# Kernel optimization log

Measured on AMD Instinct MI355X. Metric: run time of the kernel, lower is better.

## Reference

```python
import jax, jax.numpy as jnp
import numpy as np

N = 100000   # nodes
E = 3200000  # edges
C = 256      # in_channels
H = 64       # hidden_channels
G = 512      # graphs in batch
FC = [128, 64, 32, 16]
OUT = 2
EPS = 1e-5


def _linear(key, fan_in, fan_out):
    k1, k2 = jax.random.split(key)
    s = 1.0 / np.sqrt(fan_in)
    W = jax.random.uniform(k1, (fan_in, fan_out), jnp.float32, -s, s)
    b = jax.random.uniform(k2, (fan_out,), jnp.float32, -s, s)
    return W, b


def setup_inputs() -> dict:
    key = jax.random.key(0)
    ks = jax.random.split(key, 12)
    x = jax.random.normal(ks[0], (N, C), jnp.float32)
    edge_index = jax.random.randint(ks[1], (2, E), 0, N, dtype=jnp.int64)
    batch = jnp.sort(jax.random.randint(ks[2], (N,), 0, G, dtype=jnp.int64))
    w1, b1 = _linear(ks[3], C, H)
    w2, b2 = _linear(ks[4], H, H)
    g1 = jnp.ones((H,), jnp.float32); be1 = jnp.zeros((H,), jnp.float32)
    g2 = jnp.ones((H,), jnp.float32); be2 = jnp.zeros((H,), jnp.float32)
    fw1, fb1 = _linear(ks[5], H, FC[0])
    fw2, fb2 = _linear(ks[6], FC[0], FC[1])
    fw3, fb3 = _linear(ks[7], FC[1], FC[2])
    fw4, fb4 = _linear(ks[8], FC[2], FC[3])
    ow, ob = _linear(ks[9], FC[3], OUT)
    return dict(x=x, edge_index=edge_index, batch=batch,
                w1=w1, b1=b1, w2=w2, b2=b2,
                g1=g1, be1=be1, g2=g2, be2=be2,
                fw1=fw1, fb1=fb1, fw2=fw2, fb2=fb2,
                fw3=fw3, fb3=fb3, fw4=fw4, fb4=fb4,
                ow=ow, ob=ob)


def _gcn_layers(x, edge_index, w1, b1, w2, b2, g1, be1, g2, be2):
    # PyG GCNConv: add self loops, symmetric deg^-1/2 normalization, scatter-add at dst
    loops = jnp.arange(N, dtype=edge_index.dtype)
    src = jnp.concatenate([edge_index[0], loops])
    dst = jnp.concatenate([edge_index[1], loops])
    deg = jax.ops.segment_sum(jnp.ones((E + N,), jnp.float32), dst, num_segments=N)
    dis = jnp.where(deg > 0, jax.lax.rsqrt(jnp.maximum(deg, 1.0)), 0.0)
    norm = (dis[src] * dis[dst])[:, None]  # [E+N, 1]

    def conv(h, W, b):
        h = h @ W
        return jax.ops.segment_sum(h[src] * norm, dst, num_segments=N) + b

    def bn(h, g, be):  # BatchNorm1d over node dim (training-mode batch stats)
        m = jnp.mean(h, axis=0)
        v = jnp.var(h, axis=0)
        return (h - m) * jax.lax.rsqrt(v + EPS) * g + be

    h = bn(jax.nn.relu(conv(x, w1, b1)), g1, be1)   # dropout = identity (eval)
    h = bn(jax.nn.relu(conv(h, w2, b2)), g2, be2)
    return h


def reference(x, edge_index, batch, w1, b1, w2, b2, g1, be1, g2, be2,
              fw1, fb1, fw2, fb2, fw3, fb3, fw4, fb4, ow, ob):
    h = _gcn_layers(x, edge_index, w1, b1, w2, b2, g1, be1, g2, be2)
    # global_mean_pool over batch vector
    s = jax.ops.segment_sum(h, batch, num_segments=G)
    cnt = jax.ops.segment_sum(jnp.ones((N,), jnp.float32), batch, num_segments=G)
    p = s / jnp.maximum(cnt, 1.0)[:, None]  # [G, H]
    h = jax.nn.relu(p @ fw1 + fb1)
    h = jax.nn.relu(h @ fw2 + fb2)
    h = jax.nn.relu(h @ fw3 + fb3)
    h = jax.nn.relu(h @ fw4 + fb4)
    return h @ ow + ob  # [G, OUT]
```

## Files before the change

kernel.cpp:

```cpp
#include <hip/hip_runtime.h>
#include <hip/hip_fp16.h>

#define N_NODES 100000
#define E_EDGES 3200000
#define NG      512
#define BN_EPS  1e-5f

#define BSH     7
#define BNODES  128
#define NBUCK   782
#define NCHUNK  256
#define CHUNK   12500
#define DCAP    5120

__global__ __launch_bounds__(256) void k_zero(int* __restrict__ btot,
                                              float* __restrict__ stats1,
                                              float* __restrict__ stats2,
                                              float* __restrict__ sums,
                                              float* __restrict__ cnt) {
  int i = blockIdx.x * 256 + threadIdx.x;
  if (i < NBUCK) btot[i] = 0;
  if (i < 128) { stats1[i] = 0.f; stats2[i] = 0.f; }
  if (i < NG * 64) sums[i] = 0.f;
  if (i < NG) cnt[i] = 0.f;
}

__global__ __launch_bounds__(256) void kb_hist(const int* __restrict__ ei,
                                               int* __restrict__ btot) {
  __shared__ int h[NBUCK];
  const int c = blockIdx.x, tid = threadIdx.x;
  for (int b = tid; b < NBUCK; b += 256) h[b] = 0;
  __syncthreads();
  const int* dst = ei + E_EDGES + c * CHUNK;
  for (int i = tid; i < CHUNK; i += 256) atomicAdd(&h[dst[i] >> BSH], 1);
  __syncthreads();
  for (int b = tid; b < NBUCK; b += 256)
    if (h[b]) atomicAdd(&btot[b], h[b]);
}

__global__ __launch_bounds__(1024) void kb_scan2(const int* __restrict__ btot,
                                                 int* __restrict__ bbase,
                                                 int* __restrict__ cursor) {
  __shared__ int sm[1024];
  const int tid = threadIdx.x;
  const int cval = (tid < NBUCK) ? btot[tid] : 0;
  int val = cval;
  sm[tid] = val;
  __syncthreads();
  for (int off = 1; off < 1024; off <<= 1) {
    int t = (tid >= off) ? sm[tid - off] : 0;
    __syncthreads();
    val += t;
    sm[tid] = val;
    __syncthreads();
  }
  if (tid < NBUCK) { bbase[tid] = val - cval; cursor[tid] = val - cval; }
  if (tid == NBUCK - 1) bbase[NBUCK] = val;
}

__global__ __launch_bounds__(256) void kb_scatter(const int* __restrict__ ei,
                                                  int* __restrict__ cursor,
                                                  int* __restrict__ binned) {
  __shared__ int cnt[NBUCK], lcur[NBUCK], res[NBUCK];
  const int c = blockIdx.x, tid = threadIdx.x;
  for (int b = tid; b < NBUCK; b += 256) cnt[b] = 0;
  __syncthreads();
  const int* srcp = ei + c * CHUNK;
  const int* dstp = ei + E_EDGES + c * CHUNK;
  for (int i = tid; i < CHUNK; i += 256) atomicAdd(&cnt[dstp[i] >> BSH], 1);
  __syncthreads();
  for (int b = tid; b < NBUCK; b += 256) {
    res[b] = cnt[b] ? atomicAdd(&cursor[b], cnt[b]) : 0;
    lcur[b] = 0;
  }
  __syncthreads();
  for (int i = tid; i < CHUNK; i += 256) {
    const int s = srcp[i], d = dstp[i];
    const int b = d >> BSH;
    const int slot = atomicAdd(&lcur[b], 1);
    binned[res[b] + slot] = ((d & (BNODES - 1)) << 17) | s;
  }
}

__global__ __launch_bounds__(256) void kb_degsort(const int* __restrict__ binned,
                                                  const int* __restrict__ bbase,
                                                  int* __restrict__ csr,
                                                  int* __restrict__ row_start,
                                                  float* __restrict__ dis) {
  __shared__ int sA[DCAP];
  __shared__ int sB[DCAP];
  __shared__ int h[BNODES];
  __shared__ int pre[BNODES];
  __shared__ int cur[BNODES];
  const int b = blockIdx.x, tid = threadIdx.x;
  const int e0 = bbase[b], e1 = bbase[b + 1];
  const int sz = e1 - e0;
  if (tid < BNODES) h[tid] = 0;
  __syncthreads();
  if (sz <= DCAP) {
    for (int i = tid; i < sz; i += 256) {
      const int v = binned[e0 + i];
      sA[i] = v;
      atomicAdd(&h[v >> 17], 1);
    }
  } else {
    for (int i = e0 + tid; i < e1; i += 256) atomicAdd(&h[binned[i] >> 17], 1);
  }
  __syncthreads();
  if (tid < BNODES) pre[tid] = h[tid];
  __syncthreads();
  for (int off = 1; off < BNODES; off <<= 1) {
    int t = (tid >= off && tid < BNODES) ? pre[tid - off] : 0;
    __syncthreads();
    if (tid < BNODES) pre[tid] += t;
    __syncthreads();
  }
  if (tid < BNODES) {
    const int ex = pre[tid] - h[tid];
    const int n = b * BNODES + tid;
    if (n < N_NODES) {
      row_start[n] = e0 + ex;
      dis[n] = rsqrtf((float)(h[tid] + 1));
    }
    cur[tid] = ex;
  }
  if (b == NBUCK - 1 && tid == 0) row_start[N_NODES] = E_EDGES;
  __syncthreads();
  if (sz <= DCAP) {
    for (int i = tid; i < sz; i += 256) {
      const int v = sA[i];
      const int pos = atomicAdd(&cur[v >> 17], 1);
      sB[pos] = v & 0x1FFFF;
    }
    __syncthreads();
    for (int i = tid; i < sz; i += 256) csr[e0 + i] = sB[i];
  } else {
    for (int i = e0 + tid; i < e1; i += 256) {
      const int v = binned[i];
      const int pos = atomicAdd(&cur[v >> 17], 1);
      csr[e0 + pos] = v & 0x1FFFF;
    }
  }
}

template <int K, bool BN>
__global__ __launch_bounds__(256) void k_gemm(const float* __restrict__ in,
                                              const float* __restrict__ W,
                                              const float* __restrict__ dis,
                                              const float* __restrict__ stats,
                                              const float* __restrict__ gam,
                                              const float* __restrict__ bet,
                                              __half* __restrict__ y) {
  __shared__ float xs[64 * 68];
  __shared__ float wsm[64 * 64];
  __shared__ float scv[64], shv[64];
  const int tid = threadIdx.x;
  const int n0 = blockIdx.x * 64;
  const int lane = tid & 63, wv = tid >> 6;
  const int nq = lane & 15;
  const int chb = wv * 16 + (lane >> 4) * 4;
  if (BN) {
    if (tid < 64) {
      const float m = stats[tid] * (1.0f / N_NODES);
      const float v = stats[64 + tid] * (1.0f / N_NODES) - m * m;
      const float sc = rsqrtf(v + BN_EPS) * gam[tid];
      scv[tid] = sc;
      shv[tid] = bet[tid] - m * sc;
    }
  }
  float a[4][4] = {{0,0,0,0},{0,0,0,0},{0,0,0,0},{0,0,0,0}};
  for (int c0 = 0; c0 < K; c0 += 64) {
    __syncthreads();
#pragma unroll
    for (int i = 0; i < 4; ++i) {
      const int idx = tid + i * 256;
      const int n = idx >> 4, c4 = (idx & 15) * 4;
      const int nn = min(n0 + n, N_NODES - 1);
      float4 v = *(const float4*)&in[(size_t)nn * K + c0 + c4];
      if (BN) {
        v.x = v.x * scv[c4] + shv[c4];
        v.y = v.y * scv[c4 + 1] + shv[c4 + 1];
        v.z = v.z * scv[c4 + 2] + shv[c4 + 2];
        v.w = v.w * scv[c4 + 3] + shv[c4 + 3];
      }
      *(float4*)&xs[n * 68 + c4] = v;
    }
#pragma unroll
    for (int i = 0; i < 4; ++i) {
      const int idx = tid + i * 256;
      const int c = idx >> 4, ch4 = (idx & 15) * 4;
      *(float4*)&wsm[c * 64 + ch4] = *(const float4*)&W[(size_t)(c0 + c) * 64 + ch4];
    }
    __syncthreads();
    for (int c = 0; c < 64; c += 4) {
      float wq[4][4];
#pragma unroll
      for (int cc = 0; cc < 4; ++cc) {
        const float4 w4 = *(const float4*)&wsm[(c + cc) * 64 + chb];
        wq[cc][0] = w4.x; wq[cc][1] = w4.y; wq[cc][2] = w4.z; wq[cc][3] = w4.w;
      }
#pragma unroll
      for (int i = 0; i < 4; ++i) {
        const float4 xv = *(const float4*)&xs[(nq + 16 * i) * 68 + c];
#pragma unroll
        for (int j = 0; j < 4; ++j) {
          a[i][j] = fmaf(xv.x, wq[0][j],
                    fmaf(xv.y, wq[1][j],
                    fmaf(xv.z, wq[2][j],
                    fmaf(xv.w, wq[3][j], a[i][j]))));
        }
      }
    }
  }
#pragma unroll
  for (int i = 0; i < 4; ++i) {
    const int n = n0 + nq + 16 * i;
    if (n < N_NODES) {
      const float d = dis[n];
      union { __half h[4]; float2 f; } u;
      u.h[0] = __float2half_rn(d * a[i][0]);
      u.h[1] = __float2half_rn(d * a[i][1]);
      u.h[2] = __float2half_rn(d * a[i][2]);
      u.h[3] = __float2half_rn(d * a[i][3]);
      *(float2*)&y[(size_t)n * 64 + chb] = u.f;
    }
  }
}

template <bool POOL>
__global__ __launch_bounds__(256) void k_gather(const int* __restrict__ csr,
                                                const int* __restrict__ rs,
                                                const __half* __restrict__ y,
                                                const float* __restrict__ dis,
                                                const float* __restrict__ bias,
                                                float* __restrict__ hout,
                                                float* __restrict__ stats,
                                                const int* __restrict__ batch,
                                                float* __restrict__ sums,
                                                float* __restrict__ cnt) {
  const int tid = threadIdx.x;
  const int lane = tid & 63;
  const int p = lane >> 5;
  const int c = lane & 31;
  const int wid = (blockIdx.x * 256 + tid) >> 6;
  const int nw = (gridDim.x * 256) >> 6;
  const int per = (N_NODES + nw - 1) / nw;
  const int n0 = wid * per;
  const int n1 = min(N_NODES, n0 + per);
  const float bx = bias[2 * c], by = bias[2 * c + 1];
  float s1x = 0.f, s1y = 0.f, s2x = 0.f, s2y = 0.f;
  int curg = -1, run = 0;
  float px = 0.f, py = 0.f;
  for (int n = n0; n < n1; ++n) {
    int e = rs[n];
    const int end = rs[n + 1];
    float ax = 0.f, ay = 0.f;
    if (p == 0) {
      const float2 f = __half22float2(*(const __half2*)&y[(size_t)n * 64 + 2 * c]);
      ax = f.x; ay = f.y;
    }
    for (; e + 8 <= end; e += 8) {
      const int i0 = csr[e + p];
      const int i1 = csr[e + 2 + p];
      const int i2 = csr[e + 4 + p];
      const int i3 = csr[e + 6 + p];
      const float2 f0 = __half22float2(*(const __half2*)&y[(size_t)i0 * 64 + 2 * c]);
      const float2 f1 = __half22float2(*(const __half2*)&y[(size_t)i1 * 64 + 2 * c]);
      const float2 f2 = __half22float2(*(const __half2*)&y[(size_t)i2 * 64 + 2 * c]);
      const float2 f3 = __half22float2(*(const __half2*)&y[(size_t)i3 * 64 + 2 * c]);
      ax += (f0.x + f1.x) + (f2.x + f3.x);
      ay += (f0.y + f1.y) + (f2.y + f3.y);
    }
    for (; e + 2 <= end; e += 2) {
      const int i0 = csr[e + p];
      const float2 f = __half22float2(*(const __half2*)&y[(size_t)i0 * 64 + 2 * c]);
      ax += f.x; ay += f.y;
    }
    if (e < end && p == 0) {
      const int i0 = csr[e];
      const float2 f = __half22float2(*(const __half2*)&y[(size_t)i0 * 64 + 2 * c]);
      ax += f.x; ay += f.y;
    }
    ax += __shfl_xor(ax, 32);
    ay += __shfl_xor(ay, 32);
    const float d = dis[n];
    const float vx = fmaxf(d * ax + bx, 0.f);
    const float vy = fmaxf(d * ay + by, 0.f);
    if (lane < 32) {
      if (!POOL) *(float2*)&hout[(size_t)n * 64 + 2 * c] = make_float2(vx, vy);
      s1x += vx; s1y += vy;
      s2x += vx * vx; s2y += vy * vy;
    }
    if (POOL) {
      const int g = batch[n];
      if (g != curg) {
        if (run) {
          if (lane < 32) {
            atomicAdd(&sums[curg * 64 + 2 * c], px);
            atomicAdd(&sums[curg * 64 + 2 * c + 1], py);
          }
          if (lane == 0) atomicAdd(&cnt[curg], (float)run);
        }
        curg = g; run = 0; px = 0.f; py = 0.f;
      }
      if (lane < 32) { px += vx; py += vy; }
      ++run;
    }
  }
  if (POOL && run) {
    if (lane < 32) {
      atomicAdd(&sums[curg * 64 + 2 * c], px);
      atomicAdd(&sums[curg * 64 + 2 * c + 1], py);
    }
    if (lane == 0) atomicAdd(&cnt[curg], (float)run);
  }
  __shared__ float r1[256], r2[256];
  const int wv = tid >> 6;
  if (lane < 32) {
    r1[wv * 64 + 2 * c] = s1x; r1[wv * 64 + 2 * c + 1] = s1y;
    r2[wv * 64 + 2 * c] = s2x; r2[wv * 64 + 2 * c + 1] = s2y;
  }
  __syncthreads();
  if (tid < 64) {
    atomicAdd(&stats[tid], r1[tid] + r1[tid + 64] + r1[tid + 128] + r1[tid + 192]);
  } else if (tid < 128) {
    const int h = tid - 64;
    atomicAdd(&stats[64 + h], r2[h] + r2[h + 64] + r2[h + 128] + r2[h + 192]);
  }
}

__global__ __launch_bounds__(128) void k_mlp(const float* __restrict__ sums,
                                             const float* __restrict__ cnt,
                                             const float* __restrict__ stats,
                                             const float* __restrict__ gam,
                                             const float* __restrict__ bet,
                                             const float* __restrict__ fw1, const float* __restrict__ fb1,
                                             const float* __restrict__ fw2, const float* __restrict__ fb2,
                                             const float* __restrict__ fw3, const float* __restrict__ fb3,
                                             const float* __restrict__ fw4, const float* __restrict__ fb4,
                                             const float* __restrict__ ow, const float* __restrict__ ob,
                                             float* __restrict__ out) {
  __shared__ float u0[128], u1[128];
  const int g = blockIdx.x, t = threadIdx.x;
  if (t < 64) {
    const float m = stats[t] * (1.0f / N_NODES);
    const float v = stats[64 + t] * (1.0f / N_NODES) - m * m;
    const float sc = rsqrtf(v + BN_EPS) * gam[t];
    const float sh = bet[t] - m * sc;
    u0[t] = (sums[g * 64 + t] / fmaxf(cnt[g], 1.0f)) * sc + sh;
  }
  __syncthreads();
  if (t < 128) {
    float a = fb1[t];
    for (int k = 0; k < 64; ++k) a = fmaf(u0[k], fw1[k * 128 + t], a);
    u1[t] = fmaxf(a, 0.f);
  }
  __syncthreads();
  if (t < 64) {
    float a = fb2[t];
    for (int k = 0; k < 128; ++k) a = fmaf(u1[k], fw2[k * 64 + t], a);
    u0[t] = fmaxf(a, 0.f);
  }
  __syncthreads();
  if (t < 32) {
    float a = fb3[t];
    for (int k = 0; k < 64; ++k) a = fmaf(u0[k], fw3[k * 32 + t], a);
    u1[t] = fmaxf(a, 0.f);
  }
  __syncthreads();
  if (t < 16) {
    float a = fb4[t];
    for (int k = 0; k < 32; ++k) a = fmaf(u1[k], fw4[k * 16 + t], a);
    u0[t] = fmaxf(a, 0.f);
  }
  __syncthreads();
  if (t < 2) {
    float a = ob[t];
    for (int k = 0; k < 16; ++k) a = fmaf(u0[k], ow[k * 2 + t], a);
    out[g * 2 + t] = a;
  }
}

extern "C" void kernel_launch(void* const* d_in, const int* in_sizes, int n_in,
                              void* d_out, int out_size, void* d_ws, size_t ws_size,
                              hipStream_t stream) {
  const float* x    = (const float*)d_in[0];
  const int*   ei   = (const int*)d_in[1];
  const int*   batch= (const int*)d_in[2];
  const float* w1   = (const float*)d_in[3];
  const float* b1   = (const float*)d_in[4];
  const float* w2   = (const float*)d_in[5];
  const float* b2   = (const float*)d_in[6];
  const float* g1   = (const float*)d_in[7];
  const float* be1  = (const float*)d_in[8];
  const float* g2   = (const float*)d_in[9];
  const float* be2  = (const float*)d_in[10];
  const float* fw1  = (const float*)d_in[11]; const float* fb1 = (const float*)d_in[12];
  const float* fw2  = (const float*)d_in[13]; const float* fb2 = (const float*)d_in[14];
  const float* fw3  = (const float*)d_in[15]; const float* fb3 = (const float*)d_in[16];
  const float* fw4  = (const float*)d_in[17]; const float* fb4 = (const float*)d_in[18];
  const float* ow   = (const float*)d_in[19]; const float* ob  = (const float*)d_in[20];
  float* out = (float*)d_out;

  char* ws = (char*)d_ws;
  auto alloc = [&](size_t bytes) {
    void* p = ws;
    ws += (bytes + 255) & ~(size_t)255;
    return p;
  };
  float*  dis      = (float*)alloc((size_t)N_NODES * 4);
  int*    btot     = (int*)  alloc((size_t)NBUCK * 4);
  int*    bbase    = (int*)  alloc((size_t)(NBUCK + 1) * 4);
  int*    cursor   = (int*)  alloc((size_t)NBUCK * 4);
  int*    binned   = (int*)  alloc((size_t)E_EDGES * 4);
  int*    csr      = (int*)  alloc((size_t)E_EDGES * 4);
  int*    row_start= (int*)  alloc((size_t)(N_NODES + 1) * 4);
  __half* yH       = (__half*)alloc((size_t)N_NODES * 64 * 2);
  float*  hB       = (float*)alloc((size_t)N_NODES * 64 * 4);
  float*  stats1   = (float*)alloc(512);
  float*  stats2   = (float*)alloc(512);
  float*  sums     = (float*)alloc((size_t)NG * 64 * 4);
  float*  cnt      = (float*)alloc((size_t)NG * 4);

  const int nblkG = (N_NODES + 63) / 64;

  k_zero    <<<128, 256, 0, stream>>>(btot, stats1, stats2, sums, cnt);
  kb_hist   <<<NCHUNK, 256, 0, stream>>>(ei, btot);
  kb_scan2  <<<1, 1024, 0, stream>>>(btot, bbase, cursor);
  kb_scatter<<<NCHUNK, 256, 0, stream>>>(ei, cursor, binned);
  kb_degsort<<<NBUCK, 256, 0, stream>>>(binned, bbase, csr, row_start, dis);

  k_gemm<256, false><<<nblkG, 256, 0, stream>>>(x, w1, dis, nullptr, nullptr, nullptr, yH);
  k_gather<false><<<2048, 256, 0, stream>>>(csr, row_start, yH, dis, b1, hB, stats1,
                                            nullptr, nullptr, nullptr);

  k_gemm<64, true><<<nblkG, 256, 0, stream>>>(hB, w2, dis, stats1, g1, be1, yH);
  k_gather<true><<<2048, 256, 0, stream>>>(csr, row_start, yH, dis, b2, nullptr, stats2,
                                           batch, sums, cnt);

  k_mlp<<<NG, 128, 0, stream>>>(sums, cnt, stats2, g2, be2,
                                fw1, fb1, fw2, fb2, fw3, fb3, fw4, fb4, ow, ob, out);
}
```

Baseline: 610.3 us.

## Use MFMA fp16 GEMM and channel-group-major layout for gather

Moves the dense transform onto fp16 MFMA instructions, converting inputs and weights to half in shared memory. The intermediate features are stored channel-group-major (8 groups of 8 channels per node), and the gather kernel is split so each block handles one channel group, with 16 edges processed in parallel per wave. The aim is a smaller per-group working set that fits in cache during the random neighbour gather. It also halves the hidden buffer by storing it in fp16. The cost is that each edge index is reread 8 times, and precision drops for the input and hidden activations.

```diff
diff --git a/kernel.cpp b/kernel.cpp
--- a/kernel.cpp
+++ b/kernel.cpp
@@ -12,6 +12,9 @@
 #define NCHUNK  256
 #define CHUNK   12500
 #define DCAP    5120
+
+typedef _Float16 h8 __attribute__((ext_vector_type(8)));
+typedef float f4 __attribute__((ext_vector_type(4)));
 
 __global__ __launch_bounds__(256) void k_zero(int* __restrict__ btot,
                                               float* __restrict__ stats1,
@@ -144,85 +147,107 @@
 }
 
 template <int K, bool BN>
-__global__ __launch_bounds__(256) void k_gemm(const float* __restrict__ in,
+__global__ __launch_bounds__(256) void k_gemm(const void* __restrict__ in_,
                                               const float* __restrict__ W,
                                               const float* __restrict__ dis,
                                               const float* __restrict__ stats,
                                               const float* __restrict__ gam,
                                               const float* __restrict__ bet,
                                               __half* __restrict__ y) {
-  __shared__ float xs[64 * 68];
-  __shared__ float wsm[64 * 64];
+  __shared__ _Float16 xs[64 * 72];
+  __shared__ _Float16 wt[64 * 72];
   __shared__ float scv[64], shv[64];
   const int tid = threadIdx.x;
+  const int lane = tid & 63, wv = tid >> 6;
+  const int quad = lane >> 4, mrow = lane & 15;
   const int n0 = blockIdx.x * 64;
-  const int lane = tid & 63, wv = tid >> 6;
-  const int nq = lane & 15;
-  const int chb = wv * 16 + (lane >> 4) * 4;
-  if (BN) {
-    if (tid < 64) {
-      const float m = stats[tid] * (1.0f / N_NODES);
-      const float v = stats[64 + tid] * (1.0f / N_NODES) - m * m;
-      const float sc = rsqrtf(v + BN_EPS) * gam[tid];
-      scv[tid] = sc;
-      shv[tid] = bet[tid] - m * sc;
-    }
-  }
-  float a[4][4] = {{0,0,0,0},{0,0,0,0},{0,0,0,0},{0,0,0,0}};
+  if (BN && tid < 64) {
+    const float m = stats[tid] * (1.0f / N_NODES);
+    const float v = stats[64 + tid] * (1.0f / N_NODES) - m * m;
+    const float sc = rsqrtf(v + BN_EPS) * gam[tid];
+    scv[tid] = sc;
+    shv[tid] = bet[tid] - m * sc;
+  }
+  f4 acc[4];
+#pragma unroll
+  for (int t = 0; t < 4; ++t) acc[t] = (f4){0.f, 0.f, 0.f, 0.f};
+
   for (int c0 = 0; c0 < K; c0 += 64) {
     __syncthreads();
-#pragma unroll
-    for (int i = 0; i < 4; ++i) {
-      const int idx = tid + i * 256;
-      const int n = idx >> 4, c4 = (idx & 15) * 4;
+    {
+      const int n = tid >> 2, seg = (tid & 3) * 16;
       const int nn = min(n0 + n, N_NODES - 1);
-      float4 v = *(const float4*)&in[(size_t)nn * K + c0 + c4];
-      if (BN) {
-        v.x = v.x * scv[c4] + shv[c4];
-        v.y = v.y * scv[c4 + 1] + shv[c4 + 1];
-        v.z = v.z * scv[c4 + 2] + shv[c4 + 2];
-        v.w = v.w * scv[c4 + 3] + shv[c4 + 3];
-      }
-      *(float4*)&xs[n * 68 + c4] = v;
-    }
-#pragma unroll
-    for (int i = 0; i < 4; ++i) {
-      const int idx = tid + i * 256;
-      const int c = idx >> 4, ch4 = (idx & 15) * 4;
-      *(float4*)&wsm[c * 64 + ch4] = *(const float4*)&W[(size_t)(c0 + c) * 64 + ch4];
-    }
-    __syncthreads();
-    for (int c = 0; c < 64; c += 4) {
-      float wq[4][4];
-#pragma unroll
-      for (int cc = 0; cc < 4; ++cc) {
-        const float4 w4 = *(const float4*)&wsm[(c + cc) * 64 + chb];
-        wq[cc][0] = w4.x; wq[cc][1] = w4.y; wq[cc][2] = w4.z; wq[cc][3] = w4.w;
-      }
-#pragma unroll
-      for (int i = 0; i < 4; ++i) {
-        const float4 xv = *(const float4*)&xs[(nq + 16 * i) * 68 + c];
-#pragma unroll
-        for (int j = 0; j < 4; ++j) {
-          a[i][j] = fmaf(xv.x, wq[0][j],
-                    fmaf(xv.y, wq[1][j],
-                    fmaf(xv.z, wq[2][j],
-                    fmaf(xv.w, wq[3][j], a[i][j]))));
+      if (!BN) {
+        const float* src = (const float*)in_ + (size_t)nn * K + c0 + seg;
+#pragma unroll
+        for (int i = 0; i < 4; ++i) {
+          const float4 v = *(const float4*)&src[i * 4];
+          __half2 a = __floats2half2_rn(v.x, v.y);
+          __half2 b = __floats2half2_rn(v.z, v.w);
+          *(__half2*)&xs[n * 72 + seg + i * 4] = a;
+          *(__half2*)&xs[n * 72 + seg + i * 4 + 2] = b;
+        }
+      } else {
+#pragma unroll
+        for (int gg = 0; gg < 2; ++gg) {
+          const int g = (seg >> 3) + gg;
+          const __half* src = (const __half*)in_ + ((size_t)g * N_NODES + nn) * 8;
+#pragma unroll
+          for (int i = 0; i < 4; ++i) {
+            const __half2 hv = *(const __half2*)&src[i * 2];
+            const float2 f = __half22float2(hv);
+            const int ch = g * 8 + i * 2;
+            const float a = f.x * scv[ch] + shv[ch];
+            const float b = f.y * scv[ch + 1] + shv[ch + 1];
+            *(__half2*)&xs[n * 72 + ch] = __floats2half2_rn(a, b);
+          }
         }
       }
     }
-  }
-#pragma unroll
-  for (int i = 0; i < 4; ++i) {
-    const int n = n0 + nq + 16 * i;
-    if (n < N_NODES) {
-      const float d = dis[n];
-      union { __half h[4]; float2 f; } u;
-      u.h[0] = __float2half_rn(d * a[i][0]);
-      u.h[1] = __float2half_rn(d * a[i][1]);
-      u.h[2] = __float2half_rn(d * a[i][2]);
-      u.h[3] = __float2half_rn(d * a[i][3]);
-      *(float2*)&y[(size_t)n * 64 + chb] = u.f;
+    {
+      const int c = tid >> 2, seg = (tid & 3) * 16;
+      const float* src = &W[(size_t)(c0 + c) * 64 + seg];
+#pragma unroll
+      for (int i = 0; i < 4; ++i) {
+        const float4 v = *(const float4*)&src[i * 4];
+        wt[(seg + i * 4 + 0) * 72 + c] = (_Float16)v.x;
+        wt[(seg + i * 4 + 1) * 72 + c] = (_Float16)v.y;
+        wt[(seg + i * 4 + 2) * 72 + c] = (_Float16)v.z;
+        wt[(seg + i * 4 + 3) * 72 + c] = (_Float16)v.w;
+      }
+    }
+    __syncthreads();
+#pragma unroll
+    for (int ks = 0; ks < 2; ++ks) {
+      const int kb = ks * 32 + quad * 8;
+      const h8 a = *(const h8*)&xs[(wv * 16 + mrow) * 72 + kb];
+#pragma unroll
+      for (int t4 = 0; t4 < 4; ++t4) {
+        const h8 b = *(const h8*)&wt[(t4 * 16 + mrow) * 72 + kb];
+        acc[t4] = __builtin_amdgcn_mfma_f32_16x16x32_f16(a, b, acc[t4], 0, 0, 0);
+      }
+    }
+  }
+  __syncthreads();
+  _Float16* ys = xs;
+#pragma unroll
+  for (int r = 0; r < 4; ++r) {
+    const int nl = wv * 16 + quad * 4 + r;
+    const int n = n0 + nl;
+    const float d = (n < N_NODES) ? dis[n] : 0.f;
+#pragma unroll
+    for (int t4 = 0; t4 < 4; ++t4) {
+      ys[nl * 72 + t4 * 16 + mrow] = (_Float16)(d * acc[t4][r]);
+    }
+  }
+  __syncthreads();
+#pragma unroll
+  for (int rep = 0; rep < 2; ++rep) {
+    const int idx = tid + rep * 256;
+    const int g = idx & 7, n = idx >> 3;
+    const int node = n0 + n;
+    if (node < N_NODES) {
+      *(uint4*)&y[((size_t)g * N_NODES + node) * 8] = *(const uint4*)&ys[n * 72 + g * 8];
     }
   }
 }
@@ -233,100 +258,86 @@
                                                 const __half* __restrict__ y,
                                                 const float* __restrict__ dis,
                                                 const float* __restrict__ bias,
-                                                float* __restrict__ hout,
+                                                __half* __restrict__ hout,
                                                 float* __restrict__ stats,
                                                 const int* __restrict__ batch,
                                                 float* __restrict__ sums,
                                                 float* __restrict__ cnt) {
   const int tid = threadIdx.x;
-  const int lane = tid & 63;
-  const int p = lane >> 5;
-  const int c = lane & 31;
-  const int wid = (blockIdx.x * 256 + tid) >> 6;
-  const int nw = (gridDim.x * 256) >> 6;
-  const int per = (N_NODES + nw - 1) / nw;
+  const int lane = tid & 63, wv = tid >> 6;
+  const int es = lane >> 2, cd = lane & 3;
+  const int g = blockIdx.x & 7;
+  const int wid = (blockIdx.x >> 3) * 4 + wv;
+  const int nwg = (gridDim.x >> 3) * 4;
+  const int per = (N_NODES + nwg - 1) / nwg;
   const int n0 = wid * per;
   const int n1 = min(N_NODES, n0 + per);
-  const float bx = bias[2 * c], by = bias[2 * c + 1];
+  const __half* yg = y + (size_t)g * N_NODES * 8;
+  const float bx = bias[g * 8 + 2 * cd], by = bias[g * 8 + 2 * cd + 1];
   float s1x = 0.f, s1y = 0.f, s2x = 0.f, s2y = 0.f;
   int curg = -1, run = 0;
   float px = 0.f, py = 0.f;
   for (int n = n0; n < n1; ++n) {
-    int e = rs[n];
-    const int end = rs[n + 1];
+    const int e0 = rs[n], end = rs[n + 1];
     float ax = 0.f, ay = 0.f;
-    if (p == 0) {
-      const float2 f = __half22float2(*(const __half2*)&y[(size_t)n * 64 + 2 * c]);
+    if (es == 0) {
+      const float2 f = __half22float2(*(const __half2*)&yg[(size_t)n * 8 + 2 * cd]);
       ax = f.x; ay = f.y;
     }
-    for (; e + 8 <= end; e += 8) {
-      const int i0 = csr[e + p];
-      const int i1 = csr[e + 2 + p];
-      const int i2 = csr[e + 4 + p];
-      const int i3 = csr[e + 6 + p];
-      const float2 f0 = __half22float2(*(const __half2*)&y[(size_t)i0 * 64 + 2 * c]);
-      const float2 f1 = __half22float2(*(const __half2*)&y[(size_t)i1 * 64 + 2 * c]);
-      const float2 f2 = __half22float2(*(const __half2*)&y[(size_t)i2 * 64 + 2 * c]);
-      const float2 f3 = __half22float2(*(const __half2*)&y[(size_t)i3 * 64 + 2 * c]);
-      ax += (f0.x + f1.x) + (f2.x + f3.x);
-      ay += (f0.y + f1.y) + (f2.y + f3.y);
-    }
-    for (; e + 2 <= end; e += 2) {
-      const int i0 = csr[e + p];
-      const float2 f = __half22float2(*(const __half2*)&y[(size_t)i0 * 64 + 2 * c]);
+    for (int e = e0 + es; e < end; e += 16) {
+      const int s = __builtin_nontemporal_load(&csr[e]);
+      const float2 f = __half22float2(*(const __half2*)&yg[(size_t)s * 8 + 2 * cd]);
       ax += f.x; ay += f.y;
     }
-    if (e < end && p == 0) {
-      const int i0 = csr[e];
-      const float2 f = __half22float2(*(const __half2*)&y[(size_t)i0 * 64 + 2 * c]);
-      ax += f.x; ay += f.y;
-    }
-    ax += __shfl_xor(ax, 32);
-    ay += __shfl_xor(ay, 32);
+    ax += __shfl_xor(ax, 4);  ay += __shfl_xor(ay, 4);
+    ax += __shfl_xor(ax, 8);  ay += __shfl_xor(ay, 8);
+    ax += __shfl_xor(ax, 16); ay += __shfl_xor(ay, 16);
+    ax += __shfl_xor(ax, 32); ay += __shfl_xor(ay, 32);
     const float d = dis[n];
     const float vx = fmaxf(d * ax + bx, 0.f);
     const float vy = fmaxf(d * ay + by, 0.f);
-    if (lane < 32) {
-      if (!POOL) *(float2*)&hout[(size_t)n * 64 + 2 * c] = make_float2(vx, vy);
+    if (es == 0) {
+      if (!POOL) {
+        *(__half2*)&hout[((size_t)g * N_NODES + n) * 8 + 2 * cd] = __floats2half2_rn(vx, vy);
+      }
       s1x += vx; s1y += vy;
       s2x += vx * vx; s2y += vy * vy;
     }
     if (POOL) {
-      const int g = batch[n];
-      if (g != curg) {
+      const int gr = batch[n];
+      if (gr != curg) {
         if (run) {
-          if (lane < 32) {
-            atomicAdd(&sums[curg * 64 + 2 * c], px);
-            atomicAdd(&sums[curg * 64 + 2 * c + 1], py);
+          if (es == 0) {
+            atomicAdd(&sums[curg * 64 + g * 8 + 2 * cd], px);
+            atomicAdd(&sums[curg * 64 + g * 8 + 2 * cd + 1], py);
           }
-          if (lane == 0) atomicAdd(&cnt[curg], (float)run);
+          if (g == 0 && lane == 0) atomicAdd(&cnt[curg], (float)run);
         }
-        curg = g; run = 0; px = 0.f; py = 0.f;
+        curg = gr; run = 0; px = 0.f; py = 0.f;
       }
-      if (lane < 32) { px += vx; py += vy; }
+      if (es == 0) { px += vx; py += vy; }
       ++run;
     }
   }
   if (POOL && run) {
-    if (lane < 32) {
-      atomicAdd(&sums[curg * 64 + 2 * c], px);
-      atomicAdd(&sums[curg * 64 + 2 * c + 1], py);
-    }
-    if (lane == 0) atomicAdd(&cnt[curg], (float)run);
-  }
-  __shared__ float r1[256], r2[256];
-  const int wv = tid >> 6;
-  if (lane < 32) {
-    r1[wv * 64 + 2 * c] = s1x; r1[wv * 64 + 2 * c + 1] = s1y;
-    r2[wv * 64 + 2 * c] = s2x; r2[wv * 64 + 2 * c + 1] = s2y;
-  }
-  __syncthreads();
-  if (tid < 64) {
-    atomicAdd(&stats[tid], r1[tid] + r1[tid + 64] + r1[tid + 128] + r1[tid + 192]);
-  } else if (tid < 128) {
-    const int h = tid - 64;
-    atomicAdd(&stats[64 + h], r2[h] + r2[h + 64] + r2[h + 128] + r2[h + 192]);
-  }
+    if (es == 0) {
+      atomicAdd(&sums[curg * 64 + g * 8 + 2 * cd], px);
+      atomicAdd(&sums[curg * 64 + g * 8 + 2 * cd + 1], py);
+    }
+    if (g == 0 && lane == 0) atomicAdd(&cnt[curg], (float)run);
+  }
+  __shared__ float sacc[16];
+  if (tid < 16) sacc[tid] = 0.f;
+  __syncthreads();
+  if (es == 0) {
+    atomicAdd(&sacc[2 * cd], s1x);
+    atomicAdd(&sacc[2 * cd + 1], s1y);
+    atomicAdd(&sacc[8 + 2 * cd], s2x);
+    atomicAdd(&sacc[8 + 2 * cd + 1], s2y);
+  }
+  __syncthreads();
+  if (tid < 8) atomicAdd(&stats[g * 8 + tid], sacc[tid]);
+  else if (tid < 16) atomicAdd(&stats[64 + g * 8 + (tid - 8)], sacc[tid]);
 }
 
 __global__ __launch_bounds__(128) void k_mlp(const float* __restrict__ sums,
@@ -416,7 +427,7 @@
   int*    csr      = (int*)  alloc((size_t)E_EDGES * 4);
   int*    row_start= (int*)  alloc((size_t)(N_NODES + 1) * 4);
   __half* yH       = (__half*)alloc((size_t)N_NODES * 64 * 2);
-  float*  hB       = (float*)alloc((size_t)N_NODES * 64 * 4);
+  __half* hB       = (__half*)alloc((size_t)N_NODES * 64 * 2);
   float*  stats1   = (float*)alloc(512);
   float*  stats2   = (float*)alloc(512);
   float*  sums     = (float*)alloc((size_t)NG * 64 * 4);
```

Result: slower. 937.4 us (+53.6%).
